# Kernel optimization log

Measured on AMD Instinct MI355X. Metric: run time of the kernel, lower is better.

## Reference

```python
import jax, jax.numpy as jnp
import numpy as np
from jax import lax

T = 16          # timesteps
EPS = 1e-12     # torch F.normalize eps
DN = ('NCHW', 'OIHW', 'NCHW')

def conv2d(x, w, pad):
    return lax.conv_general_dilated(x, w, (1, 1), [(pad, pad), (pad, pad)],
                                    dimension_numbers=DN)

def setup_inputs() -> dict:
    key = jax.random.key(0)
    ks = jax.random.split(key, 7)
    B, C, H, W, K = 16, 512, 14, 14, 64
    return {
        'input_tensor': jax.random.normal(ks[0], (B * T, C, H, W), jnp.float32),
        'centers': jax.random.normal(ks[1], (K, C), jnp.float32) * 0.05,
        'share_w': jax.random.normal(ks[2], (K, C, 1, 1), jnp.float32) * 0.05,
        'share_b': jax.random.uniform(ks[3], (K,), jnp.float32),
        'U_z': jax.random.normal(ks[4], (K, K, 3, 3), jnp.float32) * 0.05,
        'U_r': jax.random.normal(ks[5], (K, K, 3, 3), jnp.float32) * 0.05,
        'U_h': jax.random.normal(ks[6], (K, K, 3, 3), jnp.float32) * 0.05,
    }

def reference(input_tensor, centers, share_w, share_b, U_z, U_r, U_h):
    NT, C, H, W = input_tensor.shape
    B = NT // T
    K = centers.shape[0]

    # soft-assignment pre-activation: 1x1 conv (SAME) -> [B*T, K, H, W]
    wxb = conv2d(input_tensor, share_w, 0) + share_b[None, :, None, None]
    wxb = wxb.reshape(B, T, K, H, W).transpose(1, 0, 2, 3, 4)  # [T,B,K,H,W]

    def gru_step(h, wxb_t):
        z = jax.nn.sigmoid(wxb_t + conv2d(h, U_z, 1))
        r = jax.nn.sigmoid(wxb_t + conv2d(h, U_r, 1))
        hh = jnp.tanh(wxb_t + conv2d(r * h, U_h, 1))
        h_new = (1.0 - z) * hh + z * h
        return h_new, h_new

    h0 = jnp.zeros((B, K, H, W), input_tensor.dtype)
    _, assign = lax.scan(gru_step, h0, wxb)            # [T,B,K,H,W]
    assign = assign.transpose(1, 0, 2, 3, 4).reshape(B * T, K, H * W)

    a_sum = assign.sum(-1, keepdims=True)              # [BT,K,1]
    a = a_sum * centers[None]                          # [BT,K,C]
    feats = input_tensor.reshape(B * T, C, H * W)
    x = jnp.einsum('nks,ncs->nkc', assign, feats)      # [BT,K,C]

    vlad = (x - a).reshape(B, T, K, C).sum(1)          # [B,K,C]
    vlad = vlad / jnp.maximum(jnp.linalg.norm(vlad, axis=2, keepdims=True), EPS)
    vlad = vlad.reshape(B, K * C)
    vlad = vlad / jnp.maximum(jnp.linalg.norm(vlad, axis=1, keepdims=True), EPS)
    return vlad
```

## Files before the change

### kernel.cpp

```cpp
#include <hip/hip_runtime.h>

#define Bc 16
#define Tc 16
#define Cc 512
#define Kc 64
#define Sc 196
#define KS (Kc*Sc)
#define BKS (Bc*Kc*Sc)
#define TBKS (Tc*BKS)
#define GFIN (16*64*512)
#define PART_N (8*GFIN)
#define PX 256
#define PLB2 (Kc*PX)

typedef __attribute__((ext_vector_type(8))) short bf16x8;
typedef __attribute__((ext_vector_type(4))) float f32x4;

__device__ __forceinline__ float sigmoid_f(float x) { return 1.f / (1.f + __expf(-x)); }
__device__ __forceinline__ float tanh_f(float x) { return 1.f - 2.f / (__expf(2.f * x) + 1.f); }

__device__ __forceinline__ float b2f(unsigned short u) {
    return __uint_as_float(((unsigned)u) << 16);
}
__device__ __forceinline__ unsigned short f2b(float f) {
    unsigned u = __float_as_uint(f);
    return (unsigned short)((u + 0x7FFFu + ((u >> 16) & 1u)) >> 16);
}
__device__ __forceinline__ void split1(float f, unsigned short& h, unsigned short& l) {
    unsigned u = __float_as_uint(f);
    unsigned uh = u & 0xffff0000u;
    h = (unsigned short)(uh >> 16);
    float fl = f - __uint_as_float(uh);
    l = (unsigned short)(__float_as_uint(fl) >> 16);
}

__device__ __forceinline__ float dpp_prev(float v) {
    return __int_as_float(__builtin_amdgcn_mov_dpp(__float_as_int(v), 0x111, 0xf, 0xf, true));
}
__device__ __forceinline__ float dpp_next(float v) {
    return __int_as_float(__builtin_amdgcn_mov_dpp(__float_as_int(v), 0x101, 0xf, 0xf, true));
}

__global__ __launch_bounds__(256) void k_prep_w(const float* __restrict__ w,
        unsigned short* __restrict__ wh, unsigned short* __restrict__ wl) {
    int idx = blockIdx.x * 256 + threadIdx.x;
    unsigned short h, l;
    split1(w[idx], h, l);
    wh[idx] = h; wl[idx] = l;
}

__global__ __launch_bounds__(512) void k_conv1x1(const float* __restrict__ x,
        const unsigned short* __restrict__ wh, const unsigned short* __restrict__ wl,
        const float* __restrict__ bias, float* __restrict__ wxb) {
    extern __shared__ float lds[];
    unsigned short* Xh = (unsigned short*)lds;
    unsigned short* Xl = Xh + 64 * 40;
    const int gs0 = blockIdx.x * 64;
    const int tid = threadIdx.x;
    const int wv = tid >> 6, lane = tid & 63;
    const int lg = lane >> 4, ln = lane & 15;
    const int mt = wv & 3, np = wv >> 2;
    const int colS = tid & 63, cgS = tid >> 6;
    const int gsS = gs0 + colS;
    const int nS = gsS / Sc, sS = gsS - nS * Sc;
    const float* xcol = x + (size_t)nS * (Cc * Sc) + sS;
    const int kA = np * 32 + ln;
    const float bias0 = bias[kA], bias1 = bias[kA + 16];

    f32x4 acc0 = {0.f, 0.f, 0.f, 0.f}, acc1 = {0.f, 0.f, 0.f, 0.f};
    for (int c0 = 0; c0 < Cc; c0 += 32) {
        __syncthreads();
#pragma unroll
        for (int q = 0; q < 4; ++q) {
            const int cl = cgS * 4 + q;
            unsigned short h, l;
            split1(xcol[(size_t)(c0 + cl) * Sc], h, l);
            Xh[colS * 40 + cl] = h;
            Xl[colS * 40 + cl] = l;
        }
        __syncthreads();
        bf16x8 B0h = *(const bf16x8*)(wh + (size_t)kA * Cc + c0 + lg * 8);
        bf16x8 B0l = *(const bf16x8*)(wl + (size_t)kA * Cc + c0 + lg * 8);
        bf16x8 B1h = *(const bf16x8*)(wh + (size_t)(kA + 16) * Cc + c0 + lg * 8);
        bf16x8 B1l = *(const bf16x8*)(wl + (size_t)(kA + 16) * Cc + c0 + lg * 8);
        bf16x8 Af = *(const bf16x8*)(Xh + (mt * 16 + ln) * 40 + lg * 8);
        bf16x8 Al = *(const bf16x8*)(Xl + (mt * 16 + ln) * 40 + lg * 8);
        acc0 = __builtin_amdgcn_mfma_f32_16x16x32_bf16(Af, B0h, acc0, 0, 0, 0);
        acc0 = __builtin_amdgcn_mfma_f32_16x16x32_bf16(Al, B0h, acc0, 0, 0, 0);
        acc0 = __builtin_amdgcn_mfma_f32_16x16x32_bf16(Af, B0l, acc0, 0, 0, 0);
        acc1 = __builtin_amdgcn_mfma_f32_16x16x32_bf16(Af, B1h, acc1, 0, 0, 0);
        acc1 = __builtin_amdgcn_mfma_f32_16x16x32_bf16(Al, B1h, acc1, 0, 0, 0);
        acc1 = __builtin_amdgcn_mfma_f32_16x16x32_bf16(Af, B1l, acc1, 0, 0, 0);
    }
#pragma unroll
    for (int r = 0; r < 4; ++r) {
        const int gs = gs0 + mt * 16 + lg * 4 + r;
        const int n = gs / Sc, s = gs - (gs / Sc) * Sc;
        const int t = n & 15, bb = n >> 4;
        const size_t rowbase = ((size_t)t * Bc + bb) * Kc;
        wxb[(rowbase + kA) * Sc + s] = acc0[r] + bias0;
        wxb[(rowbase + kA + 16) * Sc + s] = acc1[r] + bias1;
    }
}

__global__ __launch_bounds__(64) void k_gru_t0(const float* __restrict__ wxb,
        float* __restrict__ hplane32, unsigned short* __restrict__ hplane16,
        unsigned short* __restrict__ rhplane16, float* __restrict__ assign) {
    const int blk = blockIdx.x;
    const size_t pbase = (size_t)blk * PX;
    const size_t cbase = (size_t)blk * Sc;
    for (int i = threadIdx.x; i < PX; i += 64) {
        int row = i >> 4, col = i & 15;
        float v = 0.f;
        if (row >= 1 && row <= 14 && col >= 1 && col <= 14) {
            int s = (row - 1) * 14 + (col - 1);
            float pre = wxb[cbase + s];
            v = (1.f - sigmoid_f(pre)) * tanh_f(pre);
            assign[cbase + s] = v;
        }
        hplane32[pbase + i] = v;
        hplane16[pbase + i] = f2b(v);
        rhplane16[pbase + i] = 0;
    }
}

__global__ __launch_bounds__(512) void k_gru_gates(const unsigned short* __restrict__ hplane16,
        const float* __restrict__ wxb_t, const float* __restrict__ Uz, const float* __restrict__ Ur,
        float* __restrict__ zb, unsigned short* __restrict__ rhplane16) {
    extern __shared__ float lds[];
    unsigned short* P = (unsigned short*)lds;
    float* red = lds + 8192;
    const int b = blockIdx.x;
    const int k0 = blockIdx.y * 4;
    const int tid = threadIdx.x;
    const int wv = __builtin_amdgcn_readfirstlane(tid >> 6);
    const int lane = tid & 63;
    const int kp = wv >> 2, kiq = wv & 3;

    float preE[4]; bool valE[4]; size_t csE[4]; int kEa[4];
#pragma unroll
    for (int q = 0; q < 4; ++q) {
        const int o = tid + q * 512;
        const int set = o >> 8, px = o & 255;
        const int kp_o = set >> 2, r = set & 1;
        kEa[q] = k0 + kp_o * 2 + r;
        const int row = px >> 4, col = px & 15;
        valE[q] = (row >= 1 && row <= 14 && col >= 1 && col <= 14);
        csE[q] = ((size_t)b * Kc + kEa[q]) * Sc + (valE[q] ? (row - 1) * 14 + (col - 1) : 0);
        preE[q] = valE[q] ? wxb_t[csE[q]] : 0.f;
    }
    {
        const float4* src = (const float4*)(hplane16 + (size_t)b * PLB2);
        float4* dst = (float4*)P;
#pragma unroll
        for (int it = 0; it < 4; ++it) dst[it * 512 + tid] = src[it * 512 + tid];
    }
    __syncthreads();

    const int yp = lane >> 2, xq = (lane & 3) << 2;
    const int rowbase = (yp > 0) ? (yp - 1) : 0;
    const float* uz0 = Uz + (size_t)(k0 + kp * 2) * 576 + kiq * 144;
    const float* ur0 = Ur + (size_t)(k0 + kp * 2) * 576 + kiq * 144;
    float az[2][4] = {}, ar[2][4] = {};
    const unsigned short* Pw = P + (size_t)(kiq * 16) * PX + rowbase * 16 + xq;
#pragma unroll 2
    for (int ki = 0; ki < 16; ++ki) {
        const unsigned short* pk = Pw + ki * PX;
#pragma unroll
        for (int dy = 0; dy < 3; ++dy) {
            ushort4 u = *(const ushort4*)(pk + dy * 16);
            float4 m = make_float4(b2f(u.x), b2f(u.y), b2f(u.z), b2f(u.w));
            float e0 = dpp_prev(m.w);
            float e4 = dpp_next(m.x);
#pragma unroll
            for (int r = 0; r < 2; ++r) {
                const float* wz = uz0 + r * 576 + ki * 9 + dy * 3;
                float c0 = wz[0], c1 = wz[1], c2 = wz[2];
                az[r][0] += c0*e0  + c1*m.x + c2*m.y;
                az[r][1] += c0*m.x + c1*m.y + c2*m.z;
                az[r][2] += c0*m.y + c1*m.z + c2*m.w;
                az[r][3] += c0*m.z + c1*m.w + c2*e4;
                const float* wr = ur0 + r * 576 + ki * 9 + dy * 3;
                float d0 = wr[0], d1 = wr[1], d2 = wr[2];
                ar[r][0] += d0*e0  + d1*m.x + d2*m.y;
                ar[r][1] += d0*m.x + d1*m.y + d2*m.z;
                ar[r][2] += d0*m.y + d1*m.z + d2*m.w;
                ar[r][3] += d0*m.z + d1*m.w + d2*e4;
            }
        }
    }
    {
        float* rp = red + (size_t)wv * 1024 + lane;
#pragma unroll
        for (int r = 0; r < 2; ++r)
#pragma unroll
            for (int jj = 0; jj < 4; ++jj) {
                rp[(size_t)(r * 4 + jj) * 64] = az[r][jj];
                rp[(size_t)(8 + r * 4 + jj) * 64] = ar[r][jj];
            }
    }
    __syncthreads();
#pragma unroll
    for (int q = 0; q < 4; ++q) {
        const int o = tid + q * 512;
        const int set = o >> 8, px = o & 255;
        const int kp_o = set >> 2, g = (set >> 1) & 1, r = set & 1;
        const int lane_r = ((px >> 4) << 2) + ((px & 15) >> 2);
        const int v = (g * 2 + r) * 4 + (px & 3);
        float s0 = 0.f;
#pragma unroll
        for (int kq2 = 0; kq2 < 4; ++kq2)
            s0 += red[(size_t)((kp_o * 4 + kq2) * 16 + v) * 64 + lane_r];
        if (valE[q]) {
            float sv = sigmoid_f(preE[q] + s0);
            if (g == 0) {
                zb[csE[q]] = sv;
            } else {
                float hv = b2f(P[(size_t)kEa[q] * PX + px]);
                rhplane16[(size_t)b * PLB2 + (size_t)kEa[q] * PX + px] = f2b(sv * hv);
            }
        }
    }
}

__global__ __launch_bounds__(512) void k_gru_out(const unsigned short* __restrict__ rhplane16,
        const float* __restrict__ wxb_t, const float* __restrict__ Uh, const float* __restrict__ zb,
        float* __restrict__ hplane32, unsigned short* __restrict__ hplane16,
        float* __restrict__ assign_t) {
    extern __shared__ float lds[];
    unsigned short* P = (unsigned short*)lds;
    float* red = lds + 8192;
    const int b = blockIdx.x;
    const int k0 = blockIdx.y * 4;
    const int tid = threadIdx.x;
    const int wv = __builtin_amdgcn_readfirstlane(tid >> 6);
    const int lane = tid & 63;
    const int kp = wv >> 2, kiq = wv & 3;

    float preE[2], zvE[2], hpE[2]; bool valE[2]; size_t csE[2], ppE[2];
#pragma unroll
    for (int q = 0; q < 2; ++q) {
        const int o = tid + q * 512;
        const int set = o >> 8, px = o & 255;
        const int kp_o = set >> 1, r = set & 1;
        const int k = k0 + kp_o * 2 + r;
        const int row = px >> 4, col = px & 15;
        valE[q] = (row >= 1 && row <= 14 && col >= 1 && col <= 14);
        csE[q] = ((size_t)b * Kc + k) * Sc + (valE[q] ? (row - 1) * 14 + (col - 1) : 0);
        ppE[q] = (size_t)b * PLB2 + (size_t)k * PX + px;
        preE[q] = 0.f; zvE[q] = 0.f; hpE[q] = 0.f;
        if (valE[q]) {
            preE[q] = wxb_t[csE[q]];
            zvE[q] = zb[csE[q]];
            hpE[q] = hplane32[ppE[q]];
        }
    }
    {
        const float4* src = (const float4*)(rhplane16 + (size_t)b * PLB2);
        float4* dst = (float4*)P;
#pragma unroll
        for (int it = 0; it < 4; ++it) dst[it * 512 + tid] = src[it * 512 + tid];
    }
    __syncthreads();

    const int yp = lane >> 2, xq = (lane & 3) << 2;
    const int rowbase = (yp > 0) ? (yp - 1) : 0;
    const float* uh0 = Uh + (size_t)(k0 + kp * 2) * 576 + kiq * 144;
    float ah[2][4] = {};
    const unsigned short* Pw = P + (size_t)(kiq * 16) * PX + rowbase * 16 + xq;
#pragma unroll 2
    for (int ki = 0; ki < 16; ++ki) {
        const unsigned short* pk = Pw + ki * PX;
#pragma unroll
        for (int dy = 0; dy < 3; ++dy) {
            ushort4 u = *(const ushort4*)(pk + dy * 16);
            float4 m = make_float4(b2f(u.x), b2f(u.y), b2f(u.z), b2f(u.w));
            float e0 = dpp_prev(m.w);
            float e4 = dpp_next(m.x);
#pragma unroll
            for (int r = 0; r < 2; ++r) {
                const float* wh = uh0 + r * 576 + ki * 9 + dy * 3;
                float c0 = wh[0], c1 = wh[1], c2 = wh[2];
                ah[r][0] += c0*e0  + c1*m.x + c2*m.y;
                ah[r][1] += c0*m.x + c1*m.y + c2*m.z;
                ah[r][2] += c0*m.y + c1*m.z + c2*m.w;
                ah[r][3] += c0*m.z + c1*m.w + c2*e4;
            }
        }
    }
    {
        float* rp = red + (size_t)wv * 512 + lane;
#pragma unroll
        for (int r = 0; r < 2; ++r)
#pragma unroll
            for (int jj = 0; jj < 4; ++jj)
                rp[(size_t)(r * 4 + jj) * 64] = ah[r][jj];
    }
    __syncthreads();
#pragma unroll
    for (int q = 0; q < 2; ++q) {
        const int o = tid + q * 512;
        const int set = o >> 8, px = o & 255;
        const int kp_o = set >> 1, r = set & 1;
        const int lane_r = ((px >> 4) << 2) + ((px & 15) >> 2);
        const int v = r * 4 + (px & 3);
        float s0 = 0.f;
#pragma unroll
        for (int kq2 = 0; kq2 < 4; ++kq2)
            s0 += red[(size_t)((kp_o * 4 + kq2) * 8 + v) * 64 + lane_r];
        if (valE[q]) {
            float hh = tanh_f(preE[q] + s0);
            float hn = (1.f - zvE[q]) * hh + zvE[q] * hpE[q];
            hplane32[ppE[q]] = hn;
            hplane16[ppE[q]] = f2b(hn);
            assign_t[csE[q]] = hn;
        }
    }
}

__global__ __launch_bounds__(512) void k_einsum(const float* __restrict__ x, const float* __restrict__ assign,
                                                float* __restrict__ part) {
    extern __shared__ float lds[];
    unsigned short* Ah = (unsigned short*)lds;
    unsigned short* Al = Ah + 64 * 40;
    unsigned short* Xh = Al + 64 * 40;
    unsigned short* Xl = Xh + 128 * 40;
    const int cq = blockIdx.x, tg = blockIdx.y, b = blockIdx.z;
    const int tid = threadIdx.x;
    const int wv = tid >> 6, lane = tid & 63;
    const int lg = lane >> 4, ln = lane & 15;
    const int ka = tid >> 3, ss4 = (tid & 7) * 4;
    const int cx = tid >> 2, ss8 = (tid & 3) * 8;

    f32x4 acc[4];
#pragma unroll
    for (int mt = 0; mt < 4; ++mt) acc[mt] = (f32x4){0.f, 0.f, 0.f, 0.f};

    for (int tt = 0; tt < 2; ++tt) {
        const int t = tg * 2 + tt;
        const int n = b * Tc + t;
        const float* ap = assign + ((size_t)t * Bc + b) * KS;
        const float* xp = x + ((size_t)n * Cc + cq * 128) * Sc;
        for (int sc7 = 0; sc7 < 7; ++sc7) {
            const int s0 = sc7 * 32;
            __syncthreads();
            {
                float4 v = make_float4(0.f, 0.f, 0.f, 0.f);
                if (s0 + ss4 <= 192) v = *(const float4*)(ap + (size_t)ka * Sc + s0 + ss4);
                ushort4 h, l;
                split1(v.x, h.x, l.x); split1(v.y, h.y, l.y);
                split1(v.z, h.z, l.z); split1(v.w, h.w, l.w);
                *(ushort4*)(Ah + ka * 40 + ss4) = h;
                *(ushort4*)(Al + ka * 40 + ss4) = l;
            }
#pragma unroll
            for (int q = 0; q < 2; ++q) {
                const int so = ss8 + q * 4;
                float4 v = make_float4(0.f, 0.f, 0.f, 0.f);
                if (s0 + so <= 192) v = *(const float4*)(xp + (size_t)cx * Sc + s0 + so);
                ushort4 h, l;
                split1(v.x, h.x, l.x); split1(v.y, h.y, l.y);
                split1(v.z, h.z, l.z); split1(v.w, h.w, l.w);
                *(ushort4*)(Xh + cx * 40 + so) = h;
                *(ushort4*)(Xl + cx * 40 + so) = l;
            }
            __syncthreads();
            bf16x8 Bh = *(const bf16x8*)(Xh + (wv * 16 + ln) * 40 + lg * 8);
            bf16x8 Bl = *(const bf16x8*)(Xl + (wv * 16 + ln) * 40 + lg * 8);
#pragma unroll
            for (int mt = 0; mt < 4; ++mt) {
                bf16x8 Af = *(const bf16x8*)(Ah + (mt * 16 + ln) * 40 + lg * 8);
                bf16x8 Alo = *(const bf16x8*)(Al + (mt * 16 + ln) * 40 + lg * 8);
                acc[mt] = __builtin_amdgcn_mfma_f32_16x16x32_bf16(Af, Bh, acc[mt], 0, 0, 0);
                acc[mt] = __builtin_amdgcn_mfma_f32_16x16x32_bf16(Alo, Bh, acc[mt], 0, 0, 0);
                acc[mt] = __builtin_amdgcn_mfma_f32_16x16x32_bf16(Af, Bl, acc[mt], 0, 0, 0);
            }
        }
    }
    const int c = cq * 128 + wv * 16 + ln;
#pragma unroll
    for (int mt = 0; mt < 4; ++mt) {
#pragma unroll
        for (int r = 0; r < 4; ++r) {
            const int k = mt * 16 + lg * 4 + r;
            part[(((size_t)tg * Bc + b) * Kc + k) * Cc + c] = acc[mt][r];
        }
    }
}

__global__ __launch_bounds__(256) void k_reduce(const float* __restrict__ assign, const float* __restrict__ part,
        const float* __restrict__ centers, float* __restrict__ vlad, float* __restrict__ norm2) {
    __shared__ float redw[4];
    __shared__ float a_s;
    const int blk = blockIdx.x;
    const int b = blk >> 6, k = blk & 63;
    const int tid = threadIdx.x;
    const int wave = tid >> 6, lane = tid & 63;
    const size_t bkoff = ((size_t)b * Kc + k) * Sc;
    float s = 0.f;
    for (int q = tid; q < 784; q += 256) {
        int t = q / 49, s4 = q - t * 49;
        float4 v = *(const float4*)(assign + (size_t)t * BKS + bkoff + s4 * 4);
        s += (v.x + v.y) + (v.z + v.w);
    }
#pragma unroll
    for (int o = 1; o < 64; o <<= 1) s += __shfl_xor(s, o);
    if (lane == 0) redw[wave] = s;
    __syncthreads();
    if (tid == 0) a_s = redw[0] + redw[1] + redw[2] + redw[3];
    __syncthreads();
    const float a = a_s;
    const size_t base = ((size_t)b * Kc + k) * Cc;
    const int c = tid * 2;
    float2 acc2 = make_float2(0.f, 0.f);
#pragma unroll
    for (int g = 0; g < 8; ++g) {
        float2 p = *(const float2*)(part + (size_t)g * GFIN + base + c);
        acc2.x += p.x; acc2.y += p.y;
    }
    float2 cv = *(const float2*)(centers + (size_t)k * Cc + c);
    float v0 = acc2.x - a * cv.x, v1 = acc2.y - a * cv.y;
    *(float2*)(vlad + base + c) = make_float2(v0, v1);
    float ss = v0 * v0 + v1 * v1;
#pragma unroll
    for (int o = 1; o < 64; o <<= 1) ss += __shfl_xor(ss, o);
    __syncthreads();
    if (lane == 0) redw[wave] = ss;
    __syncthreads();
    if (tid == 0) norm2[blk] = redw[0] + redw[1] + redw[2] + redw[3];
}

__global__ __launch_bounds__(64) void k_norms(const float* __restrict__ norm2, float* __restrict__ scl) {
    const int b = blockIdx.x;
    const int k = threadIdx.x;
    float ss = norm2[b * Kc + k];
    float inv = 1.f / fmaxf(sqrtf(ss), 1e-12f);
    float g = ss * inv * inv;
#pragma unroll
    for (int o = 1; o < 64; o <<= 1) g += __shfl_xor(g, o);
    float gi = 1.f / fmaxf(sqrtf(g), 1e-12f);
    scl[b * Kc + k] = inv * gi;
}

__global__ __launch_bounds__(256) void k_scale(const float* __restrict__ vlad, const float* __restrict__ scl,
                                               float* __restrict__ out) {
    const int blk = blockIdx.x;
    const int b = blk >> 4, kt = blk & 15;
    const int tid = threadIdx.x;
    const int kk = tid >> 6, lane = tid & 63;
    const int k = kt * 4 + kk;
    const float sv = scl[b * Kc + k];
    const float* vp = vlad + ((size_t)b * Kc + k) * Cc + lane * 8;
    float* op = out + ((size_t)b * Kc + k) * Cc + lane * 8;
    float4 v0 = *(const float4*)vp;
    float4 v1 = *(const float4*)(vp + 4);
    *(float4*)op = make_float4(v0.x * sv, v0.y * sv, v0.z * sv, v0.w * sv);
    *(float4*)(op + 4) = make_float4(v1.x * sv, v1.y * sv, v1.z * sv, v1.w * sv);
}

extern "C" void kernel_launch(void* const* d_in, const int* in_sizes, int n_in,
                              void* d_out, int out_size, void* d_ws, size_t ws_size,
                              hipStream_t stream) {
    (void)in_sizes; (void)n_in; (void)out_size; (void)ws_size;
    const float* x       = (const float*)d_in[0];
    const float* centers = (const float*)d_in[1];
    const float* share_w = (const float*)d_in[2];
    const float* share_b = (const float*)d_in[3];
    const float* Uz      = (const float*)d_in[4];
    const float* Ur      = (const float*)d_in[5];
    const float* Uh      = (const float*)d_in[6];
    float* out = (float*)d_out;
    float* ws  = (float*)d_ws;

    float* part      = ws;
    float* vlad      = ws;
    float* wxb       = ws;
    unsigned short* rhplane16 = (unsigned short*)(ws + (size_t)TBKS);
    unsigned short* hplane16  = (unsigned short*)(ws + (size_t)TBKS + 131072);
    float* assign   = ws + (size_t)PART_N;
    float* zb       = assign + (size_t)TBKS;
    float* hplane32 = zb + (size_t)BKS;
    float* wreg     = hplane32 + (size_t)Bc * PLB2;
    unsigned short* w_hi = (unsigned short*)wreg;
    unsigned short* w_lo = w_hi + (size_t)Kc * Cc;
    float* norm2    = wreg + (size_t)Kc * Cc;
    float* scl      = norm2 + (size_t)Bc * Kc;

    const size_t conv_lds  = 64 * 40 * 2 * 2;
    const size_t gates_lds = 65536;
    const size_t outk_lds  = 49152;
    const size_t ein_lds   = (64 * 40 + 128 * 40) * 2 * 2;

    k_prep_w<<<dim3(128), 256, 0, stream>>>(share_w, w_hi, w_lo);
    k_conv1x1<<<dim3(784), 512, conv_lds, stream>>>(x, w_hi, w_lo, share_b, wxb);
    k_gru_t0<<<dim3(1024), 64, 0, stream>>>(wxb, hplane32, hplane16, rhplane16, assign);
    for (int t = 1; t < Tc; ++t) {
        k_gru_gates<<<dim3(16, 16), 512, gates_lds, stream>>>(hplane16, wxb + (size_t)t * BKS,
                                                              Uz, Ur, zb, rhplane16);
        k_gru_out<<<dim3(16, 16), 512, outk_lds, stream>>>(rhplane16, wxb + (size_t)t * BKS,
                                                           Uh, zb, hplane32, hplane16,
                                                           assign + (size_t)t * BKS);
    }
    k_einsum<<<dim3(4, 8, 16), 512, ein_lds, stream>>>(x, assign, part);
    k_reduce<<<dim3(Bc * Kc), 256, 0, stream>>>(assign, part, centers, vlad, norm2);
    k_norms<<<dim3(Bc), 64, 0, stream>>>(norm2, scl);
    k_scale<<<dim3(256), 256, 0, stream>>>(vlad, scl, out);
}
```

Before: 455.0 us.

## Fuse GRU t0 into conv1x1 epilogue, prefetch X into registers, swizzle LDS

Removes the separate t=0 GRU kernel by computing the first hidden state in the 1x1 conv epilogue and writing it straight into the padded h planes. A small zero-init kernel clears the planes beforehand. The conv kernel now prefetches the next channel chunk into registers before the MFMAs and uses vectorized, XOR-swizzled LDS stores to cut bank conflicts. The aim is to save a kernel launch and overlap global loads with compute, at the cost of extra registers and a separate init pass.

```diff
diff --git a/kernel.cpp b/kernel.cpp
--- a/kernel.cpp
+++ b/kernel.cpp
@@ -49,47 +49,67 @@
     wh[idx] = h; wl[idx] = l;
 }
 
+__global__ __launch_bounds__(256) void k_init(float4* __restrict__ h32,
+        float4* __restrict__ h16, float4* __restrict__ rh16) {
+    const int i = blockIdx.x * 256 + threadIdx.x;
+    const float4 z = make_float4(0.f, 0.f, 0.f, 0.f);
+    h32[i] = z;
+    if (i < 32768) { h16[i] = z; rh16[i] = z; }
+}
+
 __global__ __launch_bounds__(512) void k_conv1x1(const float* __restrict__ x,
         const unsigned short* __restrict__ wh, const unsigned short* __restrict__ wl,
-        const float* __restrict__ bias, float* __restrict__ wxb) {
-    extern __shared__ float lds[];
-    unsigned short* Xh = (unsigned short*)lds;
-    unsigned short* Xl = Xh + 64 * 40;
+        const float* __restrict__ bias, float* __restrict__ wxb,
+        float* __restrict__ assign0, float* __restrict__ hplane32,
+        unsigned short* __restrict__ hplane16) {
+    __shared__ unsigned short Xh[64 * 40];
+    __shared__ unsigned short Xl[64 * 40];
     const int gs0 = blockIdx.x * 64;
     const int tid = threadIdx.x;
     const int wv = tid >> 6, lane = tid & 63;
     const int lg = lane >> 4, ln = lane & 15;
     const int mt = wv & 3, np = wv >> 2;
-    const int colS = tid & 63, cgS = tid >> 6;
-    const int gsS = gs0 + colS;
+    const int gslS = tid & 63;
+    const int c4S = (tid >> 6) * 4;
+    const int gsS = gs0 + gslS;
     const int nS = gsS / Sc, sS = gsS - nS * Sc;
     const float* xcol = x + (size_t)nS * (Cc * Sc) + sS;
+    const int colS = (((c4S >> 3) ^ ((gslS >> 3) & 3)) << 3) + (c4S & 7);
     const int kA = np * 32 + ln;
     const float bias0 = bias[kA], bias1 = bias[kA + 16];
+    const int gsA = mt * 16 + ln;
+    const int swzA = (gsA >> 3) & 3;
+
+    float xr[4];
+#pragma unroll
+    for (int i = 0; i < 4; ++i) xr[i] = xcol[(size_t)(c4S + i) * Sc];
 
     f32x4 acc0 = {0.f, 0.f, 0.f, 0.f}, acc1 = {0.f, 0.f, 0.f, 0.f};
     for (int c0 = 0; c0 < Cc; c0 += 32) {
         __syncthreads();
-#pragma unroll
-        for (int q = 0; q < 4; ++q) {
-            const int cl = cgS * 4 + q;
-            unsigned short h, l;
-            split1(xcol[(size_t)(c0 + cl) * Sc], h, l);
-            Xh[colS * 40 + cl] = h;
-            Xl[colS * 40 + cl] = l;
+        {
+            ushort4 h, l;
+            split1(xr[0], h.x, l.x); split1(xr[1], h.y, l.y);
+            split1(xr[2], h.z, l.z); split1(xr[3], h.w, l.w);
+            *(ushort4*)(Xh + gslS * 40 + colS) = h;
+            *(ushort4*)(Xl + gslS * 40 + colS) = l;
         }
         __syncthreads();
+        if (c0 + 32 < Cc) {
+#pragma unroll
+            for (int i = 0; i < 4; ++i) xr[i] = xcol[(size_t)(c0 + 32 + c4S + i) * Sc];
+        }
         bf16x8 B0h = *(const bf16x8*)(wh + (size_t)kA * Cc + c0 + lg * 8);
         bf16x8 B0l = *(const bf16x8*)(wl + (size_t)kA * Cc + c0 + lg * 8);
         bf16x8 B1h = *(const bf16x8*)(wh + (size_t)(kA + 16) * Cc + c0 + lg * 8);
         bf16x8 B1l = *(const bf16x8*)(wl + (size_t)(kA + 16) * Cc + c0 + lg * 8);
-        bf16x8 Af = *(const bf16x8*)(Xh + (mt * 16 + ln) * 40 + lg * 8);
-        bf16x8 Al = *(const bf16x8*)(Xl + (mt * 16 + ln) * 40 + lg * 8);
+        bf16x8 Af = *(const bf16x8*)(Xh + gsA * 40 + ((lg ^ swzA) << 3));
+        bf16x8 Alo = *(const bf16x8*)(Xl + gsA * 40 + ((lg ^ swzA) << 3));
         acc0 = __builtin_amdgcn_mfma_f32_16x16x32_bf16(Af, B0h, acc0, 0, 0, 0);
-        acc0 = __builtin_amdgcn_mfma_f32_16x16x32_bf16(Al, B0h, acc0, 0, 0, 0);
+        acc0 = __builtin_amdgcn_mfma_f32_16x16x32_bf16(Alo, B0h, acc0, 0, 0, 0);
         acc0 = __builtin_amdgcn_mfma_f32_16x16x32_bf16(Af, B0l, acc0, 0, 0, 0);
         acc1 = __builtin_amdgcn_mfma_f32_16x16x32_bf16(Af, B1h, acc1, 0, 0, 0);
-        acc1 = __builtin_amdgcn_mfma_f32_16x16x32_bf16(Al, B1h, acc1, 0, 0, 0);
+        acc1 = __builtin_amdgcn_mfma_f32_16x16x32_bf16(Alo, B1h, acc1, 0, 0, 0);
         acc1 = __builtin_amdgcn_mfma_f32_16x16x32_bf16(Af, B1l, acc1, 0, 0, 0);
     }
 #pragma unroll
@@ -97,30 +117,22 @@
         const int gs = gs0 + mt * 16 + lg * 4 + r;
         const int n = gs / Sc, s = gs - (gs / Sc) * Sc;
         const int t = n & 15, bb = n >> 4;
+        const float v0 = acc0[r] + bias0;
+        const float v1 = acc1[r] + bias1;
         const size_t rowbase = ((size_t)t * Bc + bb) * Kc;
-        wxb[(rowbase + kA) * Sc + s] = acc0[r] + bias0;
-        wxb[(rowbase + kA + 16) * Sc + s] = acc1[r] + bias1;
-    }
-}
-
-__global__ __launch_bounds__(64) void k_gru_t0(const float* __restrict__ wxb,
-        float* __restrict__ hplane32, unsigned short* __restrict__ hplane16,
-        unsigned short* __restrict__ rhplane16, float* __restrict__ assign) {
-    const int blk = blockIdx.x;
-    const size_t pbase = (size_t)blk * PX;
-    const size_t cbase = (size_t)blk * Sc;
-    for (int i = threadIdx.x; i < PX; i += 64) {
-        int row = i >> 4, col = i & 15;
-        float v = 0.f;
-        if (row >= 1 && row <= 14 && col >= 1 && col <= 14) {
-            int s = (row - 1) * 14 + (col - 1);
-            float pre = wxb[cbase + s];
-            v = (1.f - sigmoid_f(pre)) * tanh_f(pre);
-            assign[cbase + s] = v;
-        }
-        hplane32[pbase + i] = v;
-        hplane16[pbase + i] = f2b(v);
-        rhplane16[pbase + i] = 0;
+        wxb[(rowbase + kA) * Sc + s] = v0;
+        wxb[(rowbase + kA + 16) * Sc + s] = v1;
+        if (t == 0) {
+            const int px = (s / 14 + 1) * 16 + (s - (s / 14) * 14 + 1);
+            const float a0 = (1.f - sigmoid_f(v0)) * tanh_f(v0);
+            const float a1 = (1.f - sigmoid_f(v1)) * tanh_f(v1);
+            assign0[((size_t)bb * Kc + kA) * Sc + s] = a0;
+            assign0[((size_t)bb * Kc + kA + 16) * Sc + s] = a1;
+            const size_t pp0 = (size_t)bb * PLB2 + (size_t)kA * PX + px;
+            const size_t pp1 = (size_t)bb * PLB2 + (size_t)(kA + 16) * PX + px;
+            hplane32[pp0] = a0; hplane16[pp0] = f2b(a0);
+            hplane32[pp1] = a1; hplane16[pp1] = f2b(a1);
+        }
     }
 }
 
@@ -486,14 +498,14 @@
     float* norm2    = wreg + (size_t)Kc * Cc;
     float* scl      = norm2 + (size_t)Bc * Kc;
 
-    const size_t conv_lds  = 64 * 40 * 2 * 2;
     const size_t gates_lds = 65536;
     const size_t outk_lds  = 49152;
     const size_t ein_lds   = (64 * 40 + 128 * 40) * 2 * 2;
 
     k_prep_w<<<dim3(128), 256, 0, stream>>>(share_w, w_hi, w_lo);
-    k_conv1x1<<<dim3(784), 512, conv_lds, stream>>>(x, w_hi, w_lo, share_b, wxb);
-    k_gru_t0<<<dim3(1024), 64, 0, stream>>>(wxb, hplane32, hplane16, rhplane16, assign);
+    k_init<<<dim3(256), 256, 0, stream>>>((float4*)hplane32, (float4*)hplane16, (float4*)rhplane16);
+    k_conv1x1<<<dim3(784), 512, 0, stream>>>(x, w_hi, w_lo, share_b, wxb,
+                                             assign, hplane32, hplane16);
     for (int t = 1; t < Tc; ++t) {
         k_gru_gates<<<dim3(16, 16), 512, gates_lds, stream>>>(hplane16, wxb + (size_t)t * BKS,
                                                               Uz, Ur, zb, rhplane16);
```

After: 456.1 us. Within noise of the previous version (+0.2%).
